# Optimization experiments

Measured on AMD Instinct MI355X. Metric: run time of the kernel, lower is better.

Reference implementation:

```python
import jax, jax.numpy as jnp
import numpy as np

B, D, LC, LQ = 16, 128, 2048, 512
NEG = -1e30


def setup_inputs() -> dict:
    key = jax.random.key(0)
    kC, kQ, k4C, k4Q, kmlu = jax.random.split(key, 5)
    return {
        "C": jax.random.normal(kC, (B, D, LC), dtype=jnp.float32),
        "Q": jax.random.normal(kQ, (B, D, LQ), dtype=jnp.float32),
        "Cmask": jnp.ones((B, LC), dtype=jnp.int32),
        "Qmask": jnp.ones((B, LQ), dtype=jnp.int32),
        "w4C": jax.random.normal(k4C, (D, 1), dtype=jnp.float32) * (6.0 / (D + 1)) ** 0.5,
        "w4Q": jax.random.normal(k4Q, (D, 1), dtype=jnp.float32) * (6.0 / (D + 1)) ** 0.5,
        "w4mlu": jax.random.normal(kmlu, (1, 1, D), dtype=jnp.float32) * (6.0 / (D + 1)) ** 0.5,
        "bias": jnp.zeros((1,), dtype=jnp.float32),
    }


def reference(C, Q, Cmask, Qmask, w4C, w4Q, w4mlu, bias):
    # C: [B, D, Lc], Q: [B, D, Lq] -> transpose to [B, L, D] as in torch forward
    Ct = jnp.transpose(C, (0, 2, 1))  # [B, Lc, D]
    Qt = jnp.transpose(Q, (0, 2, 1))  # [B, Lq, D]

    # trilinear similarity (eval mode: dropout disabled)
    sub0 = Ct @ w4C                               # [B, Lc, 1]
    sub1 = jnp.transpose(Qt @ w4Q, (0, 2, 1))     # [B, 1, Lq]
    sub2 = jnp.einsum('bcd,bqd->bcq', Ct * w4mlu, Qt)  # [B, Lc, Lq]
    S = sub0 + sub1 + sub2 + bias                 # [B, Lc, Lq]

    qm = Qmask.astype(jnp.float32)[:, None, :]    # [B, 1, Lq]
    cm = Cmask.astype(jnp.float32)[:, :, None]    # [B, Lc, 1]
    S1 = jax.nn.softmax(S + NEG * (1.0 - qm), axis=2)  # softmax over Lq
    S2 = jax.nn.softmax(S + NEG * (1.0 - cm), axis=1)  # softmax over Lc

    A = S1 @ Qt                                   # [B, Lc, D]
    Bmat = jnp.einsum('bcq,bkq->bck', S1, S2) @ Ct  # [B, Lc, D]

    out = jnp.concatenate([Ct, A, Ct * A, Ct * Bmat], axis=2)  # [B, Lc, 4D]
    return jnp.transpose(out, (0, 2, 1))          # [B, 4D, Lc]
```

## Files before the change

### kernel.cpp

```cpp
#include <hip/hip_runtime.h>
#include <math.h>

#define B_ 16
#define D_ 128
#define LC_ 2048
#define LQ_ 512
#define SHIFT_ 12.0f

typedef unsigned short ushort_t;
typedef short short8 __attribute__((ext_vector_type(8)));
typedef float f32x4 __attribute__((ext_vector_type(4)));

__device__ __forceinline__ ushort_t f2bf(float f) {
    union { float f; unsigned int u; } v; v.f = f;
    unsigned int r = (v.u + 0x7FFFu + ((v.u >> 16) & 1u)) >> 16;
    return (ushort_t)r;
}
__device__ __forceinline__ float bf2f(ushort_t h) {
    union { unsigned int u; float f; } v; v.u = ((unsigned int)h) << 16;
    return v.f;
}
__device__ __forceinline__ void gld16(const void* g, void* l) {
    __builtin_amdgcn_global_load_lds(
        (const __attribute__((address_space(1))) void*)g,
        (__attribute__((address_space(3))) void*)l, 16, 0, 0);
}
#define MFMA16(a, b, c) __builtin_amdgcn_mfma_f32_16x16x32_bf16((a), (b), (c), 0, 0, 0)

__global__ __launch_bounds__(256) void k_prep(
        const float* __restrict__ src, const float* __restrict__ scale,
        ushort_t* __restrict__ dst_cast, ushort_t* __restrict__ dst_t, int L) {
    __shared__ __align__(16) ushort_t lt[64 * 74];
    const int b = blockIdx.z, d0 = blockIdx.y * 64, l0 = blockIdx.x * 64;
    const int t = threadIdx.x;
    const int cp = t & 31;
    const int dr = t >> 5;
    const float* S = src + ((size_t)b * D_ + d0) * L + l0;
    #pragma unroll
    for (int i = 0; i < 8; ++i) {
        int d = i * 8 + dr;
        float2 v = *(const float2*)&S[(size_t)d * L + 2 * cp];
        unsigned int cpk = (unsigned int)f2bf(v.x) | ((unsigned int)f2bf(v.y) << 16);
        *(unsigned int*)(dst_cast + ((size_t)b * D_ + d0 + d) * L + l0 + 2 * cp) = cpk;
        float sc = scale ? scale[d0 + d] : 1.0f;
        unsigned int spk = (unsigned int)f2bf(v.x * sc) | ((unsigned int)f2bf(v.y * sc) << 16);
        *(unsigned int*)(lt + d * 74 + 2 * cp) = spk;
    }
    __syncthreads();
    const int c = t >> 2, dch = (t & 3) * 16;
    union { ushort_t u16[16]; uint4 u4[2]; } tmp;
    #pragma unroll
    for (int j = 0; j < 16; ++j) tmp.u16[j] = lt[(dch + j) * 74 + c];
    ushort_t* dr_ = dst_t + ((size_t)b * L + l0 + c) * D_ + d0 + dch;
    *(uint4*)dr_ = tmp.u4[0];
    *(uint4*)(dr_ + 8) = tmp.u4[1];
}

__global__ __launch_bounds__(256) void k_subs(
        const float* __restrict__ C, const float* __restrict__ Q,
        const float* __restrict__ w4C, const float* __restrict__ w4Q,
        const float* __restrict__ bias,
        float* __restrict__ sub0, float* __restrict__ sub1,
        float* __restrict__ rowZ, float* __restrict__ colZ) {
    int bid = blockIdx.x;
    const int nb0 = B_ * (LC_ / 256);
    if (bid < nb0) {
        int b = bid / (LC_ / 256);
        int c = (bid % (LC_ / 256)) * 256 + threadIdx.x;
        const float* Cb = C + (size_t)b * D_ * LC_;
        float acc = 0.f;
        #pragma unroll 8
        for (int d = 0; d < D_; ++d) acc += Cb[(size_t)d * LC_ + c] * w4C[d];
        sub0[b * LC_ + c] = acc;
        rowZ[b * LC_ + c] = 0.f;
    } else {
        int id = bid - nb0;
        int b = id / (LQ_ / 256);
        int q = (id % (LQ_ / 256)) * 256 + threadIdx.x;
        const float* Qb = Q + (size_t)b * D_ * LQ_;
        float acc = bias[0];
        #pragma unroll 8
        for (int d = 0; d < D_; ++d) acc += Qb[(size_t)d * LQ_ + q] * w4Q[d];
        sub1[b * LQ_ + q] = acc;
        colZ[b * LQ_ + q] = 0.f;
    }
}

__global__ __launch_bounds__(256) void k_score(
        const ushort_t* __restrict__ Ct_bf, const ushort_t* __restrict__ Qt_bf,
        const float* __restrict__ sub0, const float* __restrict__ sub1,
        const int* __restrict__ Cmask, const int* __restrict__ Qmask,
        ushort_t* __restrict__ E_bf, ushort_t* __restrict__ Et_bf,
        float* __restrict__ rowZ, float* __restrict__ colZ) {
    __shared__ __align__(16) ushort_t As[128 * 128];
    __shared__ __align__(16) ushort_t Bs[128 * 128];
    __shared__ float s0s[128], s1s[128], cms[128], qms[128];
    const int b = blockIdx.z, c0 = blockIdx.y * 128, q0 = blockIdx.x * 128;
    const int tid = threadIdx.x, w = tid >> 6, lane = tid & 63;
    const int l15 = lane & 15, l4 = lane >> 4;
    const int wm = w >> 1, wn = w & 1;
    if (tid < 128) {
        s0s[tid] = sub0[b * LC_ + c0 + tid];
        cms[tid] = Cmask[b * LC_ + c0 + tid] ? 1.f : 0.f;
    } else {
        int t2 = tid - 128;
        s1s[t2] = sub1[b * LQ_ + q0 + t2];
        qms[t2] = Qmask[b * LQ_ + q0 + t2] ? 1.f : 0.f;
    }
    const ushort_t* Ab = Ct_bf + ((size_t)b * LC_ + c0) * D_;
    const ushort_t* Bb = Qt_bf + ((size_t)b * LQ_ + q0) * D_;
    #pragma unroll
    for (int i = 0; i < 8; ++i) {
        int r0 = w * 32 + i * 4;
        int row = r0 + l4;
        int ch = l15 ^ (row & 7);
        gld16(Ab + (size_t)row * 128 + ch * 8, As + r0 * 128);
        gld16(Bb + (size_t)row * 128 + ch * 8, Bs + r0 * 128);
    }
    __syncthreads();
    f32x4 acc[4][4];
    const f32x4 z4 = {0.f, 0.f, 0.f, 0.f};
    #pragma unroll
    for (int i = 0; i < 4; ++i)
        #pragma unroll
        for (int j = 0; j < 4; ++j) acc[i][j] = z4;
    #pragma unroll
    for (int ks = 0; ks < 4; ++ks) {
        short8 af[4], bfr[4];
        #pragma unroll
        for (int mi = 0; mi < 4; ++mi) {
            int row = wm * 64 + mi * 16 + l15;
            int ch = (ks * 4 + l4) ^ (row & 7);
            af[mi] = *(const short8*)(As + row * 128 + ch * 8);
        }
        #pragma unroll
        for (int ni = 0; ni < 4; ++ni) {
            int row = wn * 64 + ni * 16 + l15;
            int ch = (ks * 4 + l4) ^ (row & 7);
            bfr[ni] = *(const short8*)(Bs + row * 128 + ch * 8);
        }
        #pragma unroll
        for (int mi = 0; mi < 4; ++mi)
            #pragma unroll
            for (int ni = 0; ni < 4; ++ni)
                acc[mi][ni] = MFMA16(af[mi], bfr[ni], acc[mi][ni]);
    }
    float rs[4][4];
    float cs[4] = {0.f, 0.f, 0.f, 0.f};
    #pragma unroll
    for (int mi = 0; mi < 4; ++mi)
        #pragma unroll
        for (int r = 0; r < 4; ++r) rs[mi][r] = 0.f;
    #pragma unroll
    for (int mi = 0; mi < 4; ++mi) {
        #pragma unroll
        for (int ni = 0; ni < 4; ++ni) {
            int q_l = wn * 64 + ni * 16 + l15;
            float qm = qms[q_l], s1v = s1s[q_l];
            ushort_t ets[4];
            #pragma unroll
            for (int r = 0; r < 4; ++r) {
                int c_l = wm * 64 + mi * 16 + l4 * 4 + r;
                float Sv = acc[mi][ni][r] + s0s[c_l] + s1v;
                float e = __expf(Sv - SHIFT_);
                ushort_t e1u = f2bf(e * qm);
                ushort_t e2u = f2bf(e * cms[c_l]);
                rs[mi][r] += bf2f(e1u);
                cs[ni] += bf2f(e2u);
                E_bf[((size_t)b * LC_ + c0 + c_l) * LQ_ + q0 + q_l] = e1u;
                ets[r] = e2u;
            }
            ushort4 etv = make_ushort4(ets[0], ets[1], ets[2], ets[3]);
            *(ushort4*)(Et_bf + ((size_t)b * LQ_ + q0 + q_l) * LC_ + c0 +
                        wm * 64 + mi * 16 + l4 * 4) = etv;
        }
    }
    #pragma unroll
    for (int mi = 0; mi < 4; ++mi)
        #pragma unroll
        for (int r = 0; r < 4; ++r) {
            float v = rs[mi][r];
            v += __shfl_xor(v, 1); v += __shfl_xor(v, 2);
            v += __shfl_xor(v, 4); v += __shfl_xor(v, 8);
            if (l15 == 0)
                atomicAdd(&rowZ[b * LC_ + c0 + wm * 64 + mi * 16 + l4 * 4 + r], v);
        }
    #pragma unroll
    for (int ni = 0; ni < 4; ++ni) {
        float v = cs[ni];
        v += __shfl_xor(v, 16); v += __shfl_xor(v, 32);
        if (l4 == 0)
            atomicAdd(&colZ[b * LQ_ + q0 + wn * 64 + ni * 16 + l15], v);
    }
}

__global__ __launch_bounds__(256) void k_tpart(
        const ushort_t* __restrict__ Et_bf, const ushort_t* __restrict__ Cb_bf,
        float* __restrict__ Tpart, int chunk) {
    __shared__ __align__(16) ushort_t As[128 * 64];
    __shared__ __align__(16) ushort_t Bs[128 * 64];
    const int b = blockIdx.z, sp = blockIdx.y, q0 = blockIdx.x * 128;
    const int tid = threadIdx.x, w = tid >> 6, lane = tid & 63;
    const int l15 = lane & 15, l4 = lane >> 4;
    const int l8 = lane >> 3, ch0 = lane & 7;
    const int wm = w >> 1, wn = w & 1;
    const int cbeg = sp * chunk;
    const ushort_t* Ab = Et_bf + ((size_t)b * LQ_ + q0) * LC_ + cbeg;
    const ushort_t* Bb = Cb_bf + (size_t)b * D_ * LC_ + cbeg;
    f32x4 acc[4][4];
    const f32x4 z4 = {0.f, 0.f, 0.f, 0.f};
    #pragma unroll
    for (int i = 0; i < 4; ++i)
        #pragma unroll
        for (int j = 0; j < 4; ++j) acc[i][j] = z4;
    for (int kk = 0; kk < chunk / 64; ++kk) {
        __syncthreads();
        #pragma unroll
        for (int i = 0; i < 4; ++i) {
            int r0 = w * 32 + i * 8;
            int row = r0 + l8;
            int ch = ch0 ^ (row & 7);
            gld16(Ab + (size_t)row * LC_ + kk * 64 + ch * 8, As + r0 * 64);
            gld16(Bb + (size_t)row * LC_ + kk * 64 + ch * 8, Bs + r0 * 64);
        }
        __syncthreads();
        #pragma unroll
        for (int ks = 0; ks < 2; ++ks) {
            short8 af[4], bfr[4];
            #pragma unroll
            for (int mi = 0; mi < 4; ++mi) {
                int row = wm * 64 + mi * 16 + l15;
                int ch = (ks * 4 + l4) ^ (row & 7);
                af[mi] = *(const short8*)(As + row * 64 + ch * 8);
            }
            #pragma unroll
            for (int ni = 0; ni < 4; ++ni) {
                int row = wn * 64 + ni * 16 + l15;
                int ch = (ks * 4 + l4) ^ (row & 7);
                bfr[ni] = *(const short8*)(Bs + row * 64 + ch * 8);
            }
            #pragma unroll
            for (int mi = 0; mi < 4; ++mi)
                #pragma unroll
                for (int ni = 0; ni < 4; ++ni)
                    acc[mi][ni] = MFMA16(af[mi], bfr[ni], acc[mi][ni]);
        }
    }
    float* Tp = Tpart + (((size_t)sp * B_ + b) * LQ_ + q0) * D_;
    #pragma unroll
    for (int mi = 0; mi < 4; ++mi)
        #pragma unroll
        for (int ni = 0; ni < 4; ++ni)
            #pragma unroll
            for (int r = 0; r < 4; ++r)
                Tp[(size_t)(wm * 64 + mi * 16 + l4 * 4 + r) * D_ +
                   wn * 64 + ni * 16 + l15] = acc[mi][ni][r];
}

__global__ __launch_bounds__(256) void k_treduce(
        const float* __restrict__ Tpart, const float* __restrict__ colZ,
        ushort_t* __restrict__ Tt_bf, int nsplit) {
    __shared__ __align__(16) ushort_t lt[128 * 72];
    const int b = blockIdx.y, q0 = blockIdx.x * 64;
    const int t = threadIdx.x;
    const int q = t >> 2, dp = t & 3;
    float r = 1.0f / colZ[b * LQ_ + q0 + q];
    const float4* base = (const float4*)(Tpart + ((size_t)b * LQ_ + q0 + q) * D_);
    const size_t spstr = (size_t)B_ * LQ_ * D_ / 4;
    #pragma unroll
    for (int i = 0; i < 8; ++i) {
        int d4 = dp + i * 4;
        float4 s = {0.f, 0.f, 0.f, 0.f};
        for (int sp = 0; sp < nsplit; ++sp) {
            float4 v = base[sp * spstr + d4];
            s.x += v.x; s.y += v.y; s.z += v.z; s.w += v.w;
        }
        int d = d4 * 4;
        lt[(d + 0) * 72 + q] = f2bf(s.x * r);
        lt[(d + 1) * 72 + q] = f2bf(s.y * r);
        lt[(d + 2) * 72 + q] = f2bf(s.z * r);
        lt[(d + 3) * 72 + q] = f2bf(s.w * r);
    }
    __syncthreads();
    const int d = t >> 1, half = t & 1;
    ushort_t* dst = Tt_bf + ((size_t)b * D_ + d) * LQ_ + q0 + half * 32;
    #pragma unroll
    for (int j = 0; j < 4; ++j)
        *(uint4*)(dst + j * 8) = *(const uint4*)(lt + d * 72 + half * 32 + j * 8);
}

__global__ __launch_bounds__(256) void k_out(
        const ushort_t* __restrict__ E_bf, const ushort_t* __restrict__ Qb_bf,
        const ushort_t* __restrict__ Tt_bf, const float* __restrict__ C,
        const float* __restrict__ rowZ, float* __restrict__ out) {
    __shared__ __align__(16) ushort_t Qs[128 * 64];
    __shared__ __align__(16) ushort_t Ts[128 * 64];
    __shared__ __align__(16) ushort_t Es[64 * 64];
    __shared__ float rrs[64];
    const int b = blockIdx.y, c0 = blockIdx.x * 64;
    const int tid = threadIdx.x, w = tid >> 6, lane = tid & 63;
    const int l15 = lane & 15, l4 = lane >> 4;
    const int l8 = lane >> 3, ch0 = lane & 7;
    const int wm = w >> 1, wn = w & 1;
    if (tid < 64) rrs[tid] = 1.0f / rowZ[b * LC_ + c0 + tid];
    const ushort_t* Qb = Qb_bf + (size_t)b * D_ * LQ_;
    const ushort_t* Tb = Tt_bf + (size_t)b * D_ * LQ_;
    const ushort_t* Eb = E_bf + ((size_t)b * LC_ + c0) * LQ_;
    f32x4 accA[4][2], accB[4][2];
    const f32x4 z4 = {0.f, 0.f, 0.f, 0.f};
    #pragma unroll
    for (int i = 0; i < 4; ++i)
        #pragma unroll
        for (int j = 0; j < 2; ++j) { accA[i][j] = z4; accB[i][j] = z4; }
    for (int kk = 0; kk < 8; ++kk) {
        __syncthreads();
        #pragma unroll
        for (int i = 0; i < 4; ++i) {
            int r0 = w * 32 + i * 8;
            int row = r0 + l8;
            int ch = ch0 ^ (row & 7);
            gld16(Qb + (size_t)row * LQ_ + kk * 64 + ch * 8, Qs + r0 * 64);
            gld16(Tb + (size_t)row * LQ_ + kk * 64 + ch * 8, Ts + r0 * 64);
        }
        #pragma unroll
        for (int i = 0; i < 2; ++i) {
            int r0 = w * 16 + i * 8;
            int row = r0 + l8;
            int ch = ch0 ^ (row & 7);
            gld16(Eb + (size_t)row * LQ_ + kk * 64 + ch * 8, Es + r0 * 64);
        }
        __syncthreads();
        #pragma unroll
        for (int ks = 0; ks < 2; ++ks) {
            short8 aq[4], at[4], be[2];
            #pragma unroll
            for (int mi = 0; mi < 4; ++mi) {
                int row = wm * 64 + mi * 16 + l15;
                int ch = (ks * 4 + l4) ^ (row & 7);
                aq[mi] = *(const short8*)(Qs + row * 64 + ch * 8);
                at[mi] = *(const short8*)(Ts + row * 64 + ch * 8);
            }
            #pragma unroll
            for (int ni = 0; ni < 2; ++ni) {
                int row = wn * 32 + ni * 16 + l15;
                int ch = (ks * 4 + l4) ^ (row & 7);
                be[ni] = *(const short8*)(Es + row * 64 + ch * 8);
            }
            #pragma unroll
            for (int mi = 0; mi < 4; ++mi)
                #pragma unroll
                for (int ni = 0; ni < 2; ++ni) {
                    accA[mi][ni] = MFMA16(aq[mi], be[ni], accA[mi][ni]);
                    accB[mi][ni] = MFMA16(at[mi], be[ni], accB[mi][ni]);
                }
        }
    }
    #pragma unroll
    for (int mi = 0; mi < 4; ++mi)
        #pragma unroll
        for (int ni = 0; ni < 2; ++ni) {
            int c_l = wn * 32 + ni * 16 + l15;
            int cg = c0 + c_l;
            float rr = rrs[c_l];
            #pragma unroll
            for (int r = 0; r < 4; ++r) {
                int d = wm * 64 + mi * 16 + l4 * 4 + r;
                float ct = C[((size_t)b * D_ + d) * LC_ + cg];
                float av = accA[mi][ni][r] * rr;
                float bv = accB[mi][ni][r] * rr;
                size_t o = ((size_t)b * 4 * D_ + d) * LC_ + cg;
                out[o] = ct;
                out[o + (size_t)D_ * LC_] = av;
                out[o + (size_t)2 * D_ * LC_] = ct * av;
                out[o + (size_t)3 * D_ * LC_] = ct * bv;
            }
        }
}

extern "C" void kernel_launch(void* const* d_in, const int* in_sizes, int n_in,
                              void* d_out, int out_size, void* d_ws, size_t ws_size,
                              hipStream_t stream) {
    (void)in_sizes; (void)n_in; (void)out_size;
    const float* C     = (const float*)d_in[0];
    const float* Q     = (const float*)d_in[1];
    const int*   Cmask = (const int*)d_in[2];
    const int*   Qmask = (const int*)d_in[3];
    const float* w4C   = (const float*)d_in[4];
    const float* w4Q   = (const float*)d_in[5];
    const float* w4mlu = (const float*)d_in[6];
    const float* bias  = (const float*)d_in[7];
    float* out = (float*)d_out;

    char* p = (char*)d_ws;
    auto alloc = [&](size_t bytes) -> void* {
        void* r = (void*)p; p += (bytes + 255) & ~(size_t)255; return r;
    };
    ushort_t* Ct_bf = (ushort_t*)alloc((size_t)B_ * LC_ * D_ * 2);
    ushort_t* Qt_bf = (ushort_t*)alloc((size_t)B_ * LQ_ * D_ * 2);
    ushort_t* Cb_bf = (ushort_t*)alloc((size_t)B_ * D_ * LC_ * 2);
    ushort_t* Qb_bf = (ushort_t*)alloc((size_t)B_ * D_ * LQ_ * 2);
    ushort_t* E_bf  = (ushort_t*)alloc((size_t)B_ * LC_ * LQ_ * 2);
    ushort_t* Et_bf = (ushort_t*)alloc((size_t)B_ * LQ_ * LC_ * 2);
    ushort_t* Tt_bf = (ushort_t*)alloc((size_t)B_ * D_ * LQ_ * 2);
    float* sub0 = (float*)alloc((size_t)B_ * LC_ * 4);
    float* sub1 = (float*)alloc((size_t)B_ * LQ_ * 4);
    float* rowZ = (float*)alloc((size_t)B_ * LC_ * 4);
    float* colZ = (float*)alloc((size_t)B_ * LQ_ * 4);
    size_t used = (size_t)(p - (char*)d_ws);
    size_t avail = ws_size > used ? ws_size - used : 0;
    int nsplit = 8;
    while (nsplit > 1 && (size_t)nsplit * B_ * LQ_ * D_ * 4 > avail) nsplit >>= 1;
    float* Tpart = (float*)alloc((size_t)nsplit * B_ * LQ_ * D_ * 4);
    int chunk = LC_ / nsplit;

    k_prep<<<dim3(LC_ / 64, 2, B_), 256, 0, stream>>>(C, w4mlu, Cb_bf, Ct_bf, LC_);
    k_prep<<<dim3(LQ_ / 64, 2, B_), 256, 0, stream>>>(Q, nullptr, Qb_bf, Qt_bf, LQ_);
    k_subs<<<B_ * (LC_ / 256) + B_ * (LQ_ / 256), 256, 0, stream>>>(
        C, Q, w4C, w4Q, bias, sub0, sub1, rowZ, colZ);
    k_score<<<dim3(LQ_ / 128, LC_ / 128, B_), 256, 0, stream>>>(
        Ct_bf, Qt_bf, sub0, sub1, Cmask, Qmask, E_bf, Et_bf, rowZ, colZ);
    k_tpart<<<dim3(LQ_ / 128, nsplit, B_), 256, 0, stream>>>(Et_bf, Cb_bf, Tpart, chunk);
    k_treduce<<<dim3(LQ_ / 64, B_), 256, 0, stream>>>(Tpart, colZ, Tt_bf, nsplit);
    k_out<<<dim3(LC_ / 64, B_), 256, 0, stream>>>(E_bf, Qb_bf, Tt_bf, C, rowZ, out);
}
```

Baseline: 194.1 us.

## Drop transposed exp matrix; transpose E tiles in LDS and atomically reduce T

The score kernel no longer writes a second transposed copy of the exponentiated scores. It stages the E tile in shared memory so the row-major E write is coalesced. The T-partial kernel reads row-major E, applies the context mask, and transposes into LDS itself, then accumulates into a single float buffer with atomicAdd instead of per-split partials. This removes a large bf16 write and read plus the split-reduction traffic, at the cost of scalar LDS transpose stores, many float atomics, and a memset. The split count is raised to 16.

```diff
diff --git a/kernel.cpp b/kernel.cpp
--- a/kernel.cpp
+++ b/kernel.cpp
@@ -90,10 +90,12 @@
         const ushort_t* __restrict__ Ct_bf, const ushort_t* __restrict__ Qt_bf,
         const float* __restrict__ sub0, const float* __restrict__ sub1,
         const int* __restrict__ Cmask, const int* __restrict__ Qmask,
-        ushort_t* __restrict__ E_bf, ushort_t* __restrict__ Et_bf,
+        ushort_t* __restrict__ E_bf,
         float* __restrict__ rowZ, float* __restrict__ colZ) {
-    __shared__ __align__(16) ushort_t As[128 * 128];
-    __shared__ __align__(16) ushort_t Bs[128 * 128];
+    __shared__ __align__(16) ushort_t smem[2 * 128 * 128];
+    ushort_t* As = smem;
+    ushort_t* Bs = smem + 128 * 128;
+    ushort_t* Etile = smem;
     __shared__ float s0s[128], s1s[128], cms[128], qms[128];
     const int b = blockIdx.z, c0 = blockIdx.y * 128, q0 = blockIdx.x * 128;
     const int tid = threadIdx.x, w = tid >> 6, lane = tid & 63;
@@ -145,6 +147,7 @@
             for (int ni = 0; ni < 4; ++ni)
                 acc[mi][ni] = MFMA16(af[mi], bfr[ni], acc[mi][ni]);
     }
+    __syncthreads();
     float rs[4][4];
     float cs[4] = {0.f, 0.f, 0.f, 0.f};
     #pragma unroll
@@ -157,23 +160,26 @@
         for (int ni = 0; ni < 4; ++ni) {
             int q_l = wn * 64 + ni * 16 + l15;
             float qm = qms[q_l], s1v = s1s[q_l];
-            ushort_t ets[4];
             #pragma unroll
             for (int r = 0; r < 4; ++r) {
                 int c_l = wm * 64 + mi * 16 + l4 * 4 + r;
                 float Sv = acc[mi][ni][r] + s0s[c_l] + s1v;
                 float e = __expf(Sv - SHIFT_);
                 ushort_t e1u = f2bf(e * qm);
-                ushort_t e2u = f2bf(e * cms[c_l]);
-                rs[mi][r] += bf2f(e1u);
-                cs[ni] += bf2f(e2u);
-                E_bf[((size_t)b * LC_ + c0 + c_l) * LQ_ + q0 + q_l] = e1u;
-                ets[r] = e2u;
-            }
-            ushort4 etv = make_ushort4(ets[0], ets[1], ets[2], ets[3]);
-            *(ushort4*)(Et_bf + ((size_t)b * LQ_ + q0 + q_l) * LC_ + c0 +
-                        wm * 64 + mi * 16 + l4 * 4) = etv;
-        }
+                float e1f = bf2f(e1u);
+                rs[mi][r] += e1f;
+                cs[ni] += e1f * cms[c_l];
+                Etile[c_l * 128 + (((q_l >> 3) ^ (c_l & 7)) * 8) + (q_l & 7)] = e1u;
+            }
+        }
+    }
+    __syncthreads();
+    #pragma unroll
+    for (int pass = 0; pass < 8; ++pass) {
+        int c = pass * 16 + (tid >> 4);
+        int j = tid & 15;
+        uint4 v = *(const uint4*)(Etile + c * 128 + ((j ^ (c & 7)) * 8));
+        *(uint4*)(E_bf + ((size_t)b * LC_ + c0 + c) * LQ_ + q0 + j * 8) = v;
     }
     #pragma unroll
     for (int mi = 0; mi < 4; ++mi)
@@ -195,9 +201,9 @@
 }
 
 __global__ __launch_bounds__(256) void k_tpart(
-        const ushort_t* __restrict__ Et_bf, const ushort_t* __restrict__ Cb_bf,
-        float* __restrict__ Tpart, int chunk) {
-    __shared__ __align__(16) ushort_t As[128 * 64];
+        const ushort_t* __restrict__ E_bf, const ushort_t* __restrict__ Cb_bf,
+        const int* __restrict__ Cmask, float* __restrict__ T, int chunk) {
+    __shared__ __align__(16) ushort_t At[128 * 64];
     __shared__ __align__(16) ushort_t Bs[128 * 64];
     const int b = blockIdx.z, sp = blockIdx.y, q0 = blockIdx.x * 128;
     const int tid = threadIdx.x, w = tid >> 6, lane = tid & 63;
@@ -205,8 +211,9 @@
     const int l8 = lane >> 3, ch0 = lane & 7;
     const int wm = w >> 1, wn = w & 1;
     const int cbeg = sp * chunk;
-    const ushort_t* Ab = Et_bf + ((size_t)b * LQ_ + q0) * LC_ + cbeg;
     const ushort_t* Bb = Cb_bf + (size_t)b * D_ * LC_ + cbeg;
+    const int* cm = Cmask + b * LC_;
+    const int c_l = tid >> 2, qq = tid & 3;
     f32x4 acc[4][4];
     const f32x4 z4 = {0.f, 0.f, 0.f, 0.f};
     #pragma unroll
@@ -220,8 +227,23 @@
             int r0 = w * 32 + i * 8;
             int row = r0 + l8;
             int ch = ch0 ^ (row & 7);
-            gld16(Ab + (size_t)row * LC_ + kk * 64 + ch * 8, As + r0 * 64);
             gld16(Bb + (size_t)row * LC_ + kk * 64 + ch * 8, Bs + r0 * 64);
+        }
+        {
+            int cg = cbeg + kk * 64 + c_l;
+            unsigned int keep = cm[cg] ? 0xFFFFFFFFu : 0u;
+            const ushort_t* src = E_bf + ((size_t)b * LC_ + cg) * LQ_ + q0 + qq * 32;
+            #pragma unroll
+            for (int u = 0; u < 4; ++u) {
+                union { uint4 v; ushort_t s[8]; } d;
+                d.v = *(const uint4*)(src + u * 8);
+                d.v.x &= keep; d.v.y &= keep; d.v.z &= keep; d.v.w &= keep;
+                #pragma unroll
+                for (int e = 0; e < 8; ++e) {
+                    int q = qq * 32 + u * 8 + e;
+                    At[q * 64 + (((c_l >> 3) ^ (q & 7)) * 8) + (c_l & 7)] = d.s[e];
+                }
+            }
         }
         __syncthreads();
         #pragma unroll
@@ -231,7 +253,7 @@
             for (int mi = 0; mi < 4; ++mi) {
                 int row = wm * 64 + mi * 16 + l15;
                 int ch = (ks * 4 + l4) ^ (row & 7);
-                af[mi] = *(const short8*)(As + row * 64 + ch * 8);
+                af[mi] = *(const short8*)(At + row * 64 + ch * 8);
             }
             #pragma unroll
             for (int ni = 0; ni < 4; ++ni) {
@@ -246,35 +268,30 @@
                     acc[mi][ni] = MFMA16(af[mi], bfr[ni], acc[mi][ni]);
         }
     }
-    float* Tp = Tpart + (((size_t)sp * B_ + b) * LQ_ + q0) * D_;
+    float* Tp = T + ((size_t)b * LQ_ + q0) * D_;
     #pragma unroll
     for (int mi = 0; mi < 4; ++mi)
         #pragma unroll
         for (int ni = 0; ni < 4; ++ni)
             #pragma unroll
             for (int r = 0; r < 4; ++r)
-                Tp[(size_t)(wm * 64 + mi * 16 + l4 * 4 + r) * D_ +
-                   wn * 64 + ni * 16 + l15] = acc[mi][ni][r];
+                atomicAdd(&Tp[(size_t)(wm * 64 + mi * 16 + l4 * 4 + r) * D_ +
+                              wn * 64 + ni * 16 + l15], acc[mi][ni][r]);
 }
 
 __global__ __launch_bounds__(256) void k_treduce(
-        const float* __restrict__ Tpart, const float* __restrict__ colZ,
-        ushort_t* __restrict__ Tt_bf, int nsplit) {
+        const float* __restrict__ T, const float* __restrict__ colZ,
+        ushort_t* __restrict__ Tt_bf) {
     __shared__ __align__(16) ushort_t lt[128 * 72];
     const int b = blockIdx.y, q0 = blockIdx.x * 64;
     const int t = threadIdx.x;
     const int q = t >> 2, dp = t & 3;
-    float r = 1.0f / colZ[b * LQ_ + q0 + q];
-    const float4* base = (const float4*)(Tpart + ((size_t)b * LQ_ + q0 + q) * D_);
-    const size_t spstr = (size_t)B_ * LQ_ * D_ / 4;
+    float r = 1.0f / (colZ[b * LQ_ + q0 + q] + 1e-30f);
+    const float4* base = (const float4*)(T + ((size_t)b * LQ_ + q0 + q) * D_);
     #pragma unroll
     for (int i = 0; i < 8; ++i) {
         int d4 = dp + i * 4;
-        float4 s = {0.f, 0.f, 0.f, 0.f};
-        for (int sp = 0; sp < nsplit; ++sp) {
-            float4 v = base[sp * spstr + d4];
-            s.x += v.x; s.y += v.y; s.z += v.z; s.w += v.w;
-        }
+        float4 s = base[d4];
         int d = d4 * 4;
         lt[(d + 0) * 72 + q] = f2bf(s.x * r);
         lt[(d + 1) * 72 + q] = f2bf(s.y * r);
@@ -302,7 +319,7 @@
     const int l15 = lane & 15, l4 = lane >> 4;
     const int l8 = lane >> 3, ch0 = lane & 7;
     const int wm = w >> 1, wn = w & 1;
-    if (tid < 64) rrs[tid] = 1.0f / rowZ[b * LC_ + c0 + tid];
+    if (tid < 64) rrs[tid] = 1.0f / (rowZ[b * LC_ + c0 + tid] + 1e-30f);
     const ushort_t* Qb = Qb_bf + (size_t)b * D_ * LQ_;
     const ushort_t* Tb = Tt_bf + (size_t)b * D_ * LQ_;
     const ushort_t* Eb = E_bf + ((size_t)b * LC_ + c0) * LQ_;
@@ -380,7 +397,7 @@
 extern "C" void kernel_launch(void* const* d_in, const int* in_sizes, int n_in,
                               void* d_out, int out_size, void* d_ws, size_t ws_size,
                               hipStream_t stream) {
-    (void)in_sizes; (void)n_in; (void)out_size;
+    (void)in_sizes; (void)n_in; (void)out_size; (void)ws_size;
     const float* C     = (const float*)d_in[0];
     const float* Q     = (const float*)d_in[1];
     const int*   Cmask = (const int*)d_in[2];
@@ -400,26 +417,24 @@
     ushort_t* Cb_bf = (ushort_t*)alloc((size_t)B_ * D_ * LC_ * 2);
     ushort_t* Qb_bf = (ushort_t*)alloc((size_t)B_ * D_ * LQ_ * 2);
     ushort_t* E_bf  = (ushort_t*)alloc((size_t)B_ * LC_ * LQ_ * 2);
-    ushort_t* Et_bf = (ushort_t*)alloc((size_t)B_ * LQ_ * LC_ * 2);
     ushort_t* Tt_bf = (ushort_t*)alloc((size_t)B_ * D_ * LQ_ * 2);
     float* sub0 = (float*)alloc((size_t)B_ * LC_ * 4);
     float* sub1 = (float*)alloc((size_t)B_ * LQ_ * 4);
     float* rowZ = (float*)alloc((size_t)B_ * LC_ * 4);
     float* colZ = (float*)alloc((size_t)B_ * LQ_ * 4);
-    size_t used = (size_t)(p - (char*)d_ws);
-    size_t avail = ws_size > used ? ws_size - used : 0;
-    int nsplit = 8;
-    while (nsplit > 1 && (size_t)nsplit * B_ * LQ_ * D_ * 4 > avail) nsplit >>= 1;
-    float* Tpart = (float*)alloc((size_t)nsplit * B_ * LQ_ * D_ * 4);
-    int chunk = LC_ / nsplit;
+    float* Tf   = (float*)alloc((size_t)B_ * LQ_ * D_ * 4);
+
+    const int nsplit = 16, chunk = LC_ / nsplit;
 
     k_prep<<<dim3(LC_ / 64, 2, B_), 256, 0, stream>>>(C, w4mlu, Cb_bf, Ct_bf, LC_);
     k_prep<<<dim3(LQ_ / 64, 2, B_), 256, 0, stream>>>(Q, nullptr, Qb_bf, Qt_bf, LQ_);
     k_subs<<<B_ * (LC_ / 256) + B_ * (LQ_ / 256), 256, 0, stream>>>(
         C, Q, w4C, w4Q, bias, sub0, sub1, rowZ, colZ);
+    hipMemsetAsync(Tf, 0, (size_t)B_ * LQ_ * D_ * 4, stream);
     k_score<<<dim3(LQ_ / 128, LC_ / 128, B_), 256, 0, stream>>>(
-        Ct_bf, Qt_bf, sub0, sub1, Cmask, Qmask, E_bf, Et_bf, rowZ, colZ);
-    k_tpart<<<dim3(LQ_ / 128, nsplit, B_), 256, 0, stream>>>(Et_bf, Cb_bf, Tpart, chunk);
-    k_treduce<<<dim3(LQ_ / 64, B_), 256, 0, stream>>>(Tpart, colZ, Tt_bf, nsplit);
+        Ct_bf, Qt_bf, sub0, sub1, Cmask, Qmask, E_bf, rowZ, colZ);
+    k_tpart<<<dim3(LQ_ / 128, nsplit, B_), 256, 0, stream>>>(
+        E_bf, Cb_bf, Cmask, Tf, chunk);
+    k_treduce<<<dim3(LQ_ / 64, B_), 256, 0, stream>>>(Tf, colZ, Tt_bf);
     k_out<<<dim3(LC_ / 64, B_), 256, 0, stream>>>(E_bf, Qb_bf, Tt_bf, C, rowZ, out);
 }
```

Result: slower. 224.6 us (+15.7%).
